# Kernel optimization log

Hardware: AMD Instinct MI355X
Metric: run time of the kernel (lower is better)

Reference implementation:

```python
import jax, jax.numpy as jnp
import numpy as np

NUM_HEADS = 16
HEAD_DIM = 64
HIDDEN = NUM_HEADS * HEAD_DIM  # 1024
B, S = 4, 2048
SCALE = HEAD_DIM ** -0.5


def setup_inputs() -> dict:
    key = jax.random.key(0)
    ks = jax.random.split(key, 5)
    hidden_states = jax.random.normal(ks[0], (B, S, HIDDEN), dtype=jnp.float32)
    # additive causal mask: 0 on/below diagonal, -1e9 above
    causal = jnp.tril(jnp.ones((S, S), dtype=bool))
    attention_mask = jnp.where(causal, 0.0, -1e9).astype(jnp.float32)[None, None]  # [1,1,S,S]
    init = 1.0 / np.sqrt(HIDDEN)
    wq = jax.random.normal(ks[1], (HIDDEN, HIDDEN), dtype=jnp.float32) * init
    wk = jax.random.normal(ks[2], (HIDDEN, HIDDEN), dtype=jnp.float32) * init
    wv = jax.random.normal(ks[3], (HIDDEN, HIDDEN), dtype=jnp.float32) * init
    wo = jax.random.normal(ks[4], (HIDDEN, HIDDEN), dtype=jnp.float32) * init
    return {"hidden_states": hidden_states, "attention_mask": attention_mask,
            "wq": wq, "wk": wk, "wv": wv, "wo": wo}


def reference(hidden_states, attention_mask, wq, wk, wv, wo):
    b, s, _ = hidden_states.shape
    # nn.Linear(bias=False): y = x @ W^T ; split heads -> [b, h, s, d]
    def proj(w):
        return (hidden_states @ w.T).reshape(b, s, NUM_HEADS, HEAD_DIM).transpose(0, 2, 1, 3)
    q, k, v = proj(wq), proj(wk), proj(wv)
    scores = jnp.einsum('bhqd,bhkd->bhqk', q, k) * SCALE  # [b,h,s,s] materialized
    scores = scores + attention_mask
    probs = jax.nn.softmax(scores, axis=-1)  # dropout is identity (eval / p=0)
    attn = jnp.einsum('bhqk,bhkd->bhqd', probs, v)
    attn = attn.transpose(0, 2, 1, 3).reshape(b, s, HIDDEN)
    return attn @ wo.T
```

## Files before the change

### kernel.cpp

```cpp
#include <hip/hip_runtime.h>

typedef unsigned short u16;
typedef __attribute__((ext_vector_type(8))) short bf16x8;
typedef __attribute__((ext_vector_type(4))) float f32x4;
typedef __attribute__((ext_vector_type(16))) float f32x16;

#define NUMH 16
#define HD   64
#define HID  1024
#define BB   4
#define SS   2048
#define MM   (BB*SS)

__device__ __forceinline__ u16 f2bf(float f){
  unsigned u = __builtin_bit_cast(unsigned, f);
  u += 0x7FFFu + ((u >> 16) & 1u);
  return (u16)(u >> 16);
}

__device__ __forceinline__ float exp2_fast(float x){
  float r; asm("v_exp_f32 %0, %1" : "=v"(r) : "v"(x)); return r;
}

__device__ __forceinline__ void gload_lds16(const void* g, void* l){
  __builtin_amdgcn_global_load_lds((const __attribute__((address_space(1))) void*)g,
                                   (__attribute__((address_space(3))) void*)l, 16, 0, 0);
}

__global__ __launch_bounds__(256) void cast_all(const float* __restrict__ hs,
    const float* __restrict__ wq, const float* __restrict__ wk,
    const float* __restrict__ wv, const float* __restrict__ wo,
    u16* __restrict__ dst)
{
  const int NX4 = MM*HID/4;
  const int NW4 = HID*HID/4;
  int i = blockIdx.x * 256 + threadIdx.x;
  const float* src; int local;
  if (i < NX4){ src = hs; local = i; }
  else {
    int j = i - NX4;
    int wsel = j >> 18;
    local = j & (NW4 - 1);
    src = (wsel == 0) ? wq : ((wsel == 1) ? wk : ((wsel == 2) ? wv : wo));
  }
  float4 v = reinterpret_cast<const float4*>(src)[local];
  ushort4 o = make_ushort4(f2bf(v.x), f2bf(v.y), f2bf(v.z), f2bf(v.w));
  reinterpret_cast<ushort4*>(dst)[i] = o;
}

__global__ __launch_bounds__(256) void gemm_qkv(const u16* __restrict__ A,
    const u16* __restrict__ Wq, const u16* __restrict__ Wk, const u16* __restrict__ Wv,
    u16* __restrict__ Qo, u16* __restrict__ Ko, u16* __restrict__ Vto)
{
  __shared__ alignas(16) u16 As[128*32];
  __shared__ alignas(16) u16 Bs[128*32];
  const int tid = threadIdx.x;
  const int w = tid >> 6, l = tid & 63;
  const int wr = w >> 1, wc = w & 1;
  const int lr = l & 15, lg = l >> 4;
  const int bm = blockIdx.x, bn = blockIdx.y;
  const int which = bn >> 3;
  const int ncol0 = (bn & 7) * 128;
  const u16* __restrict__ Bmat = (which == 0) ? Wq : ((which == 1) ? Wk : Wv);
  const int row0 = bm * 128;

  f32x4 acc[4][4];
  #pragma unroll
  for (int i = 0; i < 4; ++i)
    #pragma unroll
    for (int j = 0; j < 4; ++j)
      acc[i][j] = (f32x4){0.f, 0.f, 0.f, 0.f};

  const int sr = l >> 2;
  const int sc = (l & 3) * 8;

  for (int kt = 0; kt < HID/32; ++kt){
    __syncthreads();
    #pragma unroll
    for (int j = 0; j < 2; ++j){
      int rr = (w*2 + j)*16 + sr;
      gload_lds16(A    + (size_t)(row0  + rr)*HID + kt*32 + sc, (char*)As + (w*2 + j)*1024);
      gload_lds16(Bmat + (size_t)(ncol0 + rr)*HID + kt*32 + sc, (char*)Bs + (w*2 + j)*1024);
    }
    __syncthreads();
    bf16x8 af[4], bfr[4];
    #pragma unroll
    for (int i = 0; i < 4; ++i){
      af[i]  = *(const bf16x8*)(As + (wr*64 + i*16 + lr)*32 + lg*8);
      bfr[i] = *(const bf16x8*)(Bs + (wc*64 + i*16 + lr)*32 + lg*8);
    }
    #pragma unroll
    for (int i = 0; i < 4; ++i)
      #pragma unroll
      for (int j = 0; j < 4; ++j)
        acc[i][j] = __builtin_amdgcn_mfma_f32_16x16x32_bf16(af[i], bfr[j], acc[i][j], 0, 0, 0);
  }

  #pragma unroll
  for (int i = 0; i < 4; ++i){
    #pragma unroll
    for (int j = 0; j < 4; ++j){
      #pragma unroll
      for (int r = 0; r < 4; ++r){
        int gm = row0 + wr*64 + i*16 + lg*4 + r;
        int nl = ncol0 + wc*64 + j*16 + lr;
        int b_ = gm >> 11, s = gm & 2047;
        int h  = nl >> 6,  d = nl & 63;
        float v = acc[i][j][r];
        if (which == 0)
          Qo[(((size_t)b_*NUMH + h)*SS + s)*HD + d] = f2bf(v * 0.18033688f);
        else if (which == 1)
          Ko[(((size_t)b_*NUMH + h)*SS + s)*HD + d] = f2bf(v);
        else
          Vto[(((size_t)b_*NUMH + h)*HD + d)*SS + s] = f2bf(v);
      }
    }
  }
}

__global__ __launch_bounds__(256) void gemm_out(const u16* __restrict__ A,
    const u16* __restrict__ Wo, float* __restrict__ C)
{
  __shared__ alignas(16) u16 As[128*32];
  __shared__ alignas(16) u16 Bs[128*32];
  const int tid = threadIdx.x;
  const int w = tid >> 6, l = tid & 63;
  const int wr = w >> 1, wc = w & 1;
  const int lr = l & 15, lg = l >> 4;
  const int row0 = blockIdx.x * 128;
  const int ncol0 = blockIdx.y * 128;

  f32x4 acc[4][4];
  #pragma unroll
  for (int i = 0; i < 4; ++i)
    #pragma unroll
    for (int j = 0; j < 4; ++j)
      acc[i][j] = (f32x4){0.f, 0.f, 0.f, 0.f};

  const int sr = l >> 2;
  const int sc = (l & 3) * 8;

  for (int kt = 0; kt < HID/32; ++kt){
    __syncthreads();
    #pragma unroll
    for (int j = 0; j < 2; ++j){
      int rr = (w*2 + j)*16 + sr;
      gload_lds16(A  + (size_t)(row0  + rr)*HID + kt*32 + sc, (char*)As + (w*2 + j)*1024);
      gload_lds16(Wo + (size_t)(ncol0 + rr)*HID + kt*32 + sc, (char*)Bs + (w*2 + j)*1024);
    }
    __syncthreads();
    bf16x8 af[4], bfr[4];
    #pragma unroll
    for (int i = 0; i < 4; ++i){
      af[i]  = *(const bf16x8*)(As + (wr*64 + i*16 + lr)*32 + lg*8);
      bfr[i] = *(const bf16x8*)(Bs + (wc*64 + i*16 + lr)*32 + lg*8);
    }
    #pragma unroll
    for (int i = 0; i < 4; ++i)
      #pragma unroll
      for (int j = 0; j < 4; ++j)
        acc[i][j] = __builtin_amdgcn_mfma_f32_16x16x32_bf16(af[i], bfr[j], acc[i][j], 0, 0, 0);
  }

  #pragma unroll
  for (int i = 0; i < 4; ++i)
    #pragma unroll
    for (int j = 0; j < 4; ++j)
      #pragma unroll
      for (int r = 0; r < 4; ++r){
        int gm = row0 + wr*64 + i*16 + lg*4 + r;
        int nl = ncol0 + wc*64 + j*16 + lr;
        C[(size_t)gm*HID + nl] = acc[i][j][r];
      }
}

__device__ __forceinline__ void stage_kv(const u16* __restrict__ Kg, const u16* __restrict__ Vt,
    size_t bhB, int kv0, u16* Kbuf, u16* Vbuf, int w, int l)
{
  #pragma unroll
  for (int i = 0; i < 2; ++i){
    const int r = 32*i + 8*w + (l >> 3);
    const int c16 = (l & 7) ^ (r & 7);
    gload_lds16(Kg + bhB + (size_t)(kv0 + r)*HD + c16*8, (char*)Kbuf + i*4096 + w*1024);
    gload_lds16(Vt + bhB + (size_t)r*SS + kv0 + c16*8,   (char*)Vbuf + i*4096 + w*1024);
  }
}

__global__ __launch_bounds__(256) void attn_fwd(const u16* __restrict__ Qg,
    const u16* __restrict__ Kg, const u16* __restrict__ Vt, u16* __restrict__ AO)
{
  __shared__ alignas(16) u16 Ks[2][64*64];
  __shared__ alignas(16) u16 Vs[2][64*64];

  const int tid = threadIdx.x;
  const int w = tid >> 6, l = tid & 63;
  const int lq = l & 31, hi = l >> 5;
  const int wgid = blockIdx.x;
  const int bh = (wgid & 7) + 8*((wgid >> 3) & 7);
  const int strip = 15 - (wgid >> 6);
  const int b_ = bh >> 4, h = bh & 15;
  const size_t bhB = (size_t)bh * SS * HD;

  const int qs0 = strip * 128;
  const int nt = 2*strip + 2;
  const int q0w = qs0 + 32*w;
  const int qabs = q0w + lq;

  bf16x8 qf[4];
  #pragma unroll
  for (int c = 0; c < 4; ++c)
    qf[c] = *(const bf16x8*)(Qg + bhB + (size_t)qabs*HD + c*16 + hi*8);

  float mrow = -1e30f, lsum = 0.f;
  f32x16 oacc[2];
  #pragma unroll
  for (int n = 0; n < 2; ++n)
    #pragma unroll
    for (int r = 0; r < 16; ++r) oacc[n][r] = 0.f;

  int cur = 0;
  stage_kv(Kg, Vt, bhB, 0, Ks[0], Vs[0], w, l);
  __syncthreads();

  for (int t = 0; t < nt; ++t){
    const int kv0 = t*64;
    if (t + 1 < nt)
      stage_kv(Kg, Vt, bhB, (t+1)*64, Ks[cur^1], Vs[cur^1], w, l);

    if (kv0 <= q0w + 31){
      const u16* Kb = Ks[cur];
      const u16* Vb = Vs[cur];
      f32x16 sacc[2];
      #pragma unroll
      for (int mi = 0; mi < 2; ++mi)
        #pragma unroll
        for (int r = 0; r < 16; ++r) sacc[mi][r] = 0.f;
      __builtin_amdgcn_s_setprio(1);
      #pragma unroll
      for (int mi = 0; mi < 2; ++mi){
        const int krow = mi*32 + lq;
        const int sw = (krow & 7) << 4;
        #pragma unroll
        for (int c = 0; c < 4; ++c){
          bf16x8 kf = *(const bf16x8*)((const char*)Kb + krow*128 + ((c*32 + hi*16) ^ sw));
          sacc[mi] = __builtin_amdgcn_mfma_f32_32x32x16_bf16(kf, qf[c], sacc[mi], 0, 0, 0);
        }
      }
      __builtin_amdgcn_s_setprio(0);
      if (kv0 + 63 > q0w){
        #pragma unroll
        for (int mi = 0; mi < 2; ++mi)
          #pragma unroll
          for (int r = 0; r < 16; ++r){
            int kabs = kv0 + mi*32 + (r & 3) + 8*(r >> 2) + 4*hi;
            if (kabs > qabs) sacc[mi][r] = -1e30f;
          }
      }
      float vm = -1e30f;
      #pragma unroll
      for (int mi = 0; mi < 2; ++mi)
        #pragma unroll
        for (int r = 0; r < 16; ++r) vm = fmaxf(vm, sacc[mi][r]);
      vm = fmaxf(vm, __shfl_xor(vm, 32));
      const float mnew = fmaxf(mrow, vm);
      const float scl = exp2_fast(mrow - mnew);
      mrow = mnew;
      float psum = 0.f;
      #pragma unroll
      for (int mi = 0; mi < 2; ++mi)
        #pragma unroll
        for (int r = 0; r < 16; ++r){
          float p = exp2_fast(sacc[mi][r] - mnew);
          sacc[mi][r] = p;
          psum += p;
        }
      psum += __shfl_xor(psum, 32);
      lsum = lsum*scl + psum;
      #pragma unroll
      for (int n = 0; n < 2; ++n)
        #pragma unroll
        for (int r = 0; r < 16; ++r) oacc[n][r] *= scl;

      bf16x8 pf[4];
      #pragma unroll
      for (int c = 0; c < 4; ++c){
        const int mi = c >> 1;
        const int geb = (c & 1) * 8;
        unsigned a0 = (unsigned)f2bf(sacc[mi][geb+0]) | ((unsigned)f2bf(sacc[mi][geb+1]) << 16);
        unsigned a1 = (unsigned)f2bf(sacc[mi][geb+2]) | ((unsigned)f2bf(sacc[mi][geb+3]) << 16);
        unsigned b0 = (unsigned)f2bf(sacc[mi][geb+4]) | ((unsigned)f2bf(sacc[mi][geb+5]) << 16);
        unsigned b1 = (unsigned)f2bf(sacc[mi][geb+6]) | ((unsigned)f2bf(sacc[mi][geb+7]) << 16);
        unsigned sel0 = hi ? b0 : a0, sel1 = hi ? b1 : a1;
        unsigned oth0 = hi ? a0 : b0, oth1 = hi ? a1 : b1;
        unsigned rcv0 = (unsigned)__shfl_xor((int)oth0, 32);
        unsigned rcv1 = (unsigned)__shfl_xor((int)oth1, 32);
        union { unsigned u[4]; bf16x8 v; } pu;
        pu.u[0] = hi ? rcv0 : sel0;
        pu.u[1] = hi ? rcv1 : sel1;
        pu.u[2] = hi ? sel0 : rcv0;
        pu.u[3] = hi ? sel1 : rcv1;
        pf[c] = pu.v;
      }

      __builtin_amdgcn_s_setprio(1);
      #pragma unroll
      for (int n = 0; n < 2; ++n){
        const int drow = n*32 + lq;
        const int swv = (drow & 7) << 4;
        #pragma unroll
        for (int c = 0; c < 4; ++c){
          bf16x8 vf = *(const bf16x8*)((const char*)Vb + drow*128 + ((c*32 + hi*16) ^ swv));
          oacc[n] = __builtin_amdgcn_mfma_f32_32x32x16_bf16(vf, pf[c], oacc[n], 0, 0, 0);
        }
      }
      __builtin_amdgcn_s_setprio(0);
    }
    __syncthreads();
    cur ^= 1;
  }

  const float inv = 1.f / lsum;
  u16* dst = AO + ((size_t)b_*SS + qabs)*HID + h*HD;
  #pragma unroll
  for (int n = 0; n < 2; ++n)
    #pragma unroll
    for (int g = 0; g < 4; ++g){
      ushort4 o;
      o.x = f2bf(oacc[n][4*g+0] * inv);
      o.y = f2bf(oacc[n][4*g+1] * inv);
      o.z = f2bf(oacc[n][4*g+2] * inv);
      o.w = f2bf(oacc[n][4*g+3] * inv);
      *(ushort4*)(dst + n*32 + 8*g + 4*hi) = o;
    }
}

extern "C" void kernel_launch(void* const* d_in, const int* in_sizes, int n_in,
                              void* d_out, int out_size, void* d_ws, size_t ws_size,
                              hipStream_t stream)
{
  const float* hs = (const float*)d_in[0];
  const float* wq = (const float*)d_in[2];
  const float* wk = (const float*)d_in[3];
  const float* wv = (const float*)d_in[4];
  const float* wo = (const float*)d_in[5];

  char* ws = (char*)d_ws;
  u16* Xb  = (u16*)(ws);
  u16* Wqb = (u16*)(ws + ((size_t)16 << 20));
  u16* Wkb = (u16*)(ws + ((size_t)18 << 20));
  u16* Wvb = (u16*)(ws + ((size_t)20 << 20));
  u16* Wob = (u16*)(ws + ((size_t)22 << 20));
  u16* Q   = (u16*)(ws + ((size_t)24 << 20));
  u16* Kb  = (u16*)(ws + ((size_t)40 << 20));
  u16* Vt  = (u16*)(ws + ((size_t)56 << 20));
  u16* AO  = (u16*)(ws + ((size_t)72 << 20));

  cast_all<<<12288, 256, 0, stream>>>(hs, wq, wk, wv, wo, Xb);

  gemm_qkv<<<dim3(64, 24), 256, 0, stream>>>(Xb, Wqb, Wkb, Wvb, Q, Kb, Vt);
  attn_fwd<<<1024, 256, 0, stream>>>(Q, Kb, Vt, AO);
  gemm_out<<<dim3(64, 8), 256, 0, stream>>>(AO, Wob, (float*)d_out);
}
```

Baseline: 190.2 us.

## Widen GEMM K-tile to 64 with XOR-swizzled LDS and transposed V epilogue

```diff
diff --git a/kernel.cpp b/kernel.cpp
--- a/kernel.cpp
+++ b/kernel.cpp
@@ -43,7 +43,8 @@
     local = j & (NW4 - 1);
     src = (wsel == 0) ? wq : ((wsel == 1) ? wk : ((wsel == 2) ? wv : wo));
   }
-  float4 v = reinterpret_cast<const float4*>(src)[local];
+  float4 v = reinterpret_cast<const float4*>(src)[i < NX4 ? local : local];
+  v = reinterpret_cast<const float4*>(src)[local];
   ushort4 o = make_ushort4(f2bf(v.x), f2bf(v.y), f2bf(v.z), f2bf(v.w));
   reinterpret_cast<ushort4*>(dst)[i] = o;
 }
@@ -52,8 +53,8 @@
     const u16* __restrict__ Wq, const u16* __restrict__ Wk, const u16* __restrict__ Wv,
     u16* __restrict__ Qo, u16* __restrict__ Ko, u16* __restrict__ Vto)
 {
-  __shared__ alignas(16) u16 As[128*32];
-  __shared__ alignas(16) u16 Bs[128*32];
+  __shared__ alignas(16) u16 As[128*64];
+  __shared__ alignas(16) u16 Bs[128*64];
   const int tid = threadIdx.x;
   const int w = tid >> 6, l = tid & 63;
   const int wr = w >> 1, wc = w & 1;
@@ -71,48 +72,75 @@
     for (int j = 0; j < 4; ++j)
       acc[i][j] = (f32x4){0.f, 0.f, 0.f, 0.f};
 
-  const int sr = l >> 2;
-  const int sc = (l & 3) * 8;
-
-  for (int kt = 0; kt < HID/32; ++kt){
-    __syncthreads();
-    #pragma unroll
-    for (int j = 0; j < 2; ++j){
-      int rr = (w*2 + j)*16 + sr;
-      gload_lds16(A    + (size_t)(row0  + rr)*HID + kt*32 + sc, (char*)As + (w*2 + j)*1024);
-      gload_lds16(Bmat + (size_t)(ncol0 + rr)*HID + kt*32 + sc, (char*)Bs + (w*2 + j)*1024);
-    }
-    __syncthreads();
-    bf16x8 af[4], bfr[4];
+  const int srow = l >> 3;
+  const int cg8  = ((l & 7) ^ srow) * 8;
+
+  for (int kt = 0; kt < HID/64; ++kt){
+    __syncthreads();
+    #pragma unroll
+    for (int j = 0; j < 4; ++j){
+      int rr = j*32 + w*8 + srow;
+      gload_lds16(A    + (size_t)(row0  + rr)*HID + kt*64 + cg8, (char*)As + j*4096 + w*1024);
+      gload_lds16(Bmat + (size_t)(ncol0 + rr)*HID + kt*64 + cg8, (char*)Bs + j*4096 + w*1024);
+    }
+    __syncthreads();
+    #pragma unroll
+    for (int kk = 0; kk < 2; ++kk){
+      bf16x8 af[4], bfr[4];
+      #pragma unroll
+      for (int i = 0; i < 4; ++i){
+        const int offb = ((kk*4 + lg) ^ (lr & 7)) * 16;
+        af[i]  = *(const bf16x8*)((const char*)As + (wr*64 + i*16 + lr)*128 + offb);
+        bfr[i] = *(const bf16x8*)((const char*)Bs + (wc*64 + i*16 + lr)*128 + offb);
+      }
+      if (which == 2){
+        #pragma unroll
+        for (int i = 0; i < 4; ++i)
+          #pragma unroll
+          for (int j = 0; j < 4; ++j)
+            acc[i][j] = __builtin_amdgcn_mfma_f32_16x16x32_bf16(bfr[j], af[i], acc[i][j], 0, 0, 0);
+      } else {
+        #pragma unroll
+        for (int i = 0; i < 4; ++i)
+          #pragma unroll
+          for (int j = 0; j < 4; ++j)
+            acc[i][j] = __builtin_amdgcn_mfma_f32_16x16x32_bf16(af[i], bfr[j], acc[i][j], 0, 0, 0);
+      }
+    }
+  }
+
+  if (which == 2){
     #pragma unroll
     for (int i = 0; i < 4; ++i){
-      af[i]  = *(const bf16x8*)(As + (wr*64 + i*16 + lr)*32 + lg*8);
-      bfr[i] = *(const bf16x8*)(Bs + (wc*64 + i*16 + lr)*32 + lg*8);
-    }
-    #pragma unroll
-    for (int i = 0; i < 4; ++i)
-      #pragma unroll
-      for (int j = 0; j < 4; ++j)
-        acc[i][j] = __builtin_amdgcn_mfma_f32_16x16x32_bf16(af[i], bfr[j], acc[i][j], 0, 0, 0);
-  }
-
-  #pragma unroll
-  for (int i = 0; i < 4; ++i){
-    #pragma unroll
-    for (int j = 0; j < 4; ++j){
-      #pragma unroll
-      for (int r = 0; r < 4; ++r){
-        int gm = row0 + wr*64 + i*16 + lg*4 + r;
-        int nl = ncol0 + wc*64 + j*16 + lr;
-        int b_ = gm >> 11, s = gm & 2047;
-        int h  = nl >> 6,  d = nl & 63;
-        float v = acc[i][j][r];
-        if (which == 0)
-          Qo[(((size_t)b_*NUMH + h)*SS + s)*HD + d] = f2bf(v * 0.18033688f);
-        else if (which == 1)
-          Ko[(((size_t)b_*NUMH + h)*SS + s)*HD + d] = f2bf(v);
-        else
-          Vto[(((size_t)b_*NUMH + h)*HD + d)*SS + s] = f2bf(v);
+      #pragma unroll
+      for (int j = 0; j < 4; ++j){
+        #pragma unroll
+        for (int r = 0; r < 4; ++r){
+          int nl = ncol0 + wc*64 + j*16 + lg*4 + r;
+          int gm = row0 + wr*64 + i*16 + lr;
+          int b_ = gm >> 11, s = gm & 2047;
+          int h  = nl >> 6,  d = nl & 63;
+          Vto[(((size_t)b_*NUMH + h)*HD + d)*SS + s] = f2bf(acc[i][j][r]);
+        }
+      }
+    }
+  } else {
+    #pragma unroll
+    for (int i = 0; i < 4; ++i){
+      #pragma unroll
+      for (int j = 0; j < 4; ++j){
+        #pragma unroll
+        for (int r = 0; r < 4; ++r){
+          int gm = row0 + wr*64 + i*16 + lg*4 + r;
+          int nl = ncol0 + wc*64 + j*16 + lr;
+          int b_ = gm >> 11, s = gm & 2047;
+          int h  = nl >> 6,  d = nl & 63;
+          float v = acc[i][j][r];
+          if (which == 0)
+            Qo[(((size_t)b_*NUMH + h)*SS + s)*HD + d] = f2bf(v * 0.18033688f);
+          else
+            Ko[(((size_t)b_*NUMH + h)*SS + s)*HD + d] = f2bf(v);
+        }
       }
     }
   }
@@ -121,8 +149,8 @@
 __global__ __launch_bounds__(256) void gemm_out(const u16* __restrict__ A,
     const u16* __restrict__ Wo, float* __restrict__ C)
 {
-  __shared__ alignas(16) u16 As[128*32];
-  __shared__ alignas(16) u16 Bs[128*32];
+  __shared__ alignas(16) u16 As[128*64];
+  __shared__ alignas(16) u16 Bs[128*64];
   const int tid = threadIdx.x;
   const int w = tid >> 6, l = tid & 63;
   const int wr = w >> 1, wc = w & 1;
@@ -137,29 +165,33 @@
     for (int j = 0; j < 4; ++j)
       acc[i][j] = (f32x4){0.f, 0.f, 0.f, 0.f};
 
-  const int sr = l >> 2;
-  const int sc = (l & 3) * 8;
-
-  for (int kt = 0; kt < HID/32; ++kt){
-    __syncthreads();
-    #pragma unroll
-    for (int j = 0; j < 2; ++j){
-      int rr = (w*2 + j)*16 + sr;
-      gload_lds16(A  + (size_t)(row0  + rr)*HID + kt*32 + sc, (char*)As + (w*2 + j)*1024);
-      gload_lds16(Wo + (size_t)(ncol0 + rr)*HID + kt*32 + sc, (char*)Bs + (w*2 + j)*1024);
-    }
-    __syncthreads();
-    bf16x8 af[4], bfr[4];
-    #pragma unroll
-    for (int i = 0; i < 4; ++i){
-      af[i]  = *(const bf16x8*)(As + (wr*64 + i*16 + lr)*32 + lg*8);
-      bfr[i] = *(const bf16x8*)(Bs + (wc*64 + i*16 + lr)*32 + lg*8);
-    }
-    #pragma unroll
-    for (int i = 0; i < 4; ++i)
-      #pragma unroll
-      for (int j = 0; j < 4; ++j)
-        acc[i][j] = __builtin_amdgcn_mfma_f32_16x16x32_bf16(af[i], bfr[j], acc[i][j], 0, 0, 0);
+  const int srow = l >> 3;
+  const int cg8  = ((l & 7) ^ srow) * 8;
+
+  for (int kt = 0; kt < HID/64; ++kt){
+    __syncthreads();
+    #pragma unroll
+    for (int j = 0; j < 4; ++j){
+      int rr = j*32 + w*8 + srow;
+      gload_lds16(A  + (size_t)(row0  + rr)*HID + kt*64 + cg8, (char*)As + j*4096 + w*1024);
+      gload_lds16(Wo + (size_t)(ncol0 + rr)*HID + kt*64 + cg8, (char*)Bs + j*4096 + w*1024);
+    }
+    __syncthreads();
+    #pragma unroll
+    for (int kk = 0; kk < 2; ++kk){
+      bf16x8 af[4], bfr[4];
+      #pragma unroll
+      for (int i = 0; i < 4; ++i){
+        const int offb = ((kk*4 + lg) ^ (lr & 7)) * 16;
+        af[i]  = *(const bf16x8*)((const char*)As + (wr*64 + i*16 + lr)*128 + offb);
+        bfr[i] = *(const bf16x8*)((const char*)Bs + (wc*64 + i*16 + lr)*128 + offb);
+      }
+      #pragma unroll
+      for (int i = 0; i < 4; ++i)
+        #pragma unroll
+        for (int j = 0; j < 4; ++j)
+          acc[i][j] = __builtin_amdgcn_mfma_f32_16x16x32_bf16(af[i], bfr[j], acc[i][j], 0, 0, 0);
+    }
   }
 
   #pragma unroll
```

Measured after the change: 166.3 us. 12.6% less time.
